# Kernel tuning notes

Hardware: AMD Instinct MI355X
Metric: run time of the kernel (lower is better)

Reference implementation:

```python
import jax, jax.numpy as jnp
import numpy as np

B, NQ, NKV = 4, 1024, 2048
DQ, DC, DI, H = 1024, 1024, 1024, 16
DH = DI // H
EPS = 1e-5


def layer_norm(x, gamma, beta):
    mu = jnp.mean(x, axis=-1, keepdims=True)
    var = jnp.var(x, axis=-1, keepdims=True)
    return (x - mu) * jax.lax.rsqrt(var + EPS) * gamma + beta


def setup_inputs() -> dict:
    key = jax.random.key(0)
    ks = jax.random.split(key, 6)
    s = 0.02
    return {
        "q": jax.random.normal(ks[0], (B, NQ, DQ), jnp.float32),
        "context": jax.random.normal(ks[1], (B, NKV, DC), jnp.float32),
        "Wq": jax.random.normal(ks[2], (DI, DQ), jnp.float32) * s,
        "Wkv": jax.random.normal(ks[3], (2 * DI, DC), jnp.float32) * s,
        "Wproj": jax.random.normal(ks[4], (DQ, DI), jnp.float32) * s,
        "bproj": jnp.zeros((DQ,), jnp.float32),
        "q_gamma": jnp.ones((DQ,), jnp.float32),
        "q_beta": jnp.zeros((DQ,), jnp.float32),
        "c_gamma": jnp.ones((DC,), jnp.float32),
        "c_beta": jnp.zeros((DC,), jnp.float32),
    }


def reference(q, context, Wq, Wkv, Wproj, bproj, q_gamma, q_beta, c_gamma, c_beta):
    scale = DH ** -0.5
    qn = layer_norm(q, q_gamma, q_beta)            # [b, nq, dq]
    cn = layer_norm(context, c_gamma, c_beta)      # [b, nkv, dc]
    qp = qn @ Wq.T                                  # [b, nq, di]
    kv = cn @ Wkv.T                                 # [b, nkv, 2*di]
    k, v = kv[..., :DI], kv[..., DI:]
    qh = qp.reshape(B, NQ, H, DH)
    kh = k.reshape(B, NKV, H, DH)
    vh = v.reshape(B, NKV, H, DH)
    attn = jnp.einsum('bnhd,bmhd->bhnm', qh, kh) * scale   # [b,h,nq,nkv]
    attn = jax.nn.softmax(attn, axis=-1)
    out = jnp.einsum('bhnm,bmhd->bnhd', attn, vh).reshape(B, NQ, DI)
    return out @ Wproj.T + bproj
```

## Files before the change

### kernel.cpp

```cpp
#include <hip/hip_runtime.h>
#include <hip/hip_bf16.h>
#include <stdint.h>

#define B_N 4
#define NQ 1024
#define NKV 2048
#define DI 1024
#define H 16
#define DH 64

using bf16 = __bf16;
typedef bf16 bf16x8 __attribute__((ext_vector_type(8)));
typedef bf16 bf16x4 __attribute__((ext_vector_type(4)));
typedef float f32x4 __attribute__((ext_vector_type(4)));

typedef const __attribute__((address_space(1))) void* gptr_t;
typedef __attribute__((address_space(3))) void* sptr_t;

__global__ __launch_bounds__(256) void prep_kernel(
    const float* __restrict__ q, const float* __restrict__ ctx,
    const float* __restrict__ qg, const float* __restrict__ qb,
    const float* __restrict__ cg, const float* __restrict__ cb,
    bf16* __restrict__ qn, bf16* __restrict__ cn,
    const float* __restrict__ Wq, const float* __restrict__ Wkv, const float* __restrict__ Wproj,
    bf16* __restrict__ oq, bf16* __restrict__ okv, bf16* __restrict__ op) {
  const int blk = blockIdx.x;
  const int t = threadIdx.x;
  if (blk >= 12288) {
    int i = (blk - 12288) * 256 + t;
    const float* src; bf16* dst; int j;
    if (i < 262144)      { src = Wq;    dst = oq;  j = i; }
    else if (i < 786432) { src = Wkv;   dst = okv; j = i - 262144; }
    else                 { src = Wproj; dst = op;  j = i - 786432; }
    float4 v = reinterpret_cast<const float4*>(src)[j];
    bf16x4 o;
    o[0] = (bf16)v.x; o[1] = (bf16)v.y; o[2] = (bf16)v.z; o[3] = (bf16)v.w;
    reinterpret_cast<bf16x4*>(dst)[j] = o;
    return;
  }
  const float* x; const float* gamma; const float* beta; bf16* out; int r;
  if (blk < 4096) { x = q;   gamma = qg; beta = qb; out = qn; r = blk; }
  else            { x = ctx; gamma = cg; beta = cb; out = cn; r = blk - 4096; }
  const float4 v = reinterpret_cast<const float4*>(x + (size_t)r * 1024)[t];
  float s = v.x + v.y + v.z + v.w;
  float s2 = v.x*v.x + v.y*v.y + v.z*v.z + v.w*v.w;
#pragma unroll
  for (int m = 1; m < 64; m <<= 1) { s += __shfl_xor(s, m); s2 += __shfl_xor(s2, m); }
  __shared__ float red[8];
  int wid = t >> 6;
  if ((t & 63) == 0) { red[wid] = s; red[wid + 4] = s2; }
  __syncthreads();
  float ts  = red[0] + red[1] + red[2] + red[3];
  float ts2 = red[4] + red[5] + red[6] + red[7];
  float mean = ts * (1.0f / 1024.0f);
  float var  = ts2 * (1.0f / 1024.0f) - mean * mean;
  float rstd = rsqrtf(var + 1e-5f);
  float4 g  = reinterpret_cast<const float4*>(gamma)[t];
  float4 bb = reinterpret_cast<const float4*>(beta)[t];
  bf16x4 o;
  o[0] = (bf16)((v.x - mean) * rstd * g.x + bb.x);
  o[1] = (bf16)((v.y - mean) * rstd * g.y + bb.y);
  o[2] = (bf16)((v.z - mean) * rstd * g.z + bb.z);
  o[3] = (bf16)((v.w - mean) * rstd * g.w + bb.w);
  reinterpret_cast<bf16x4*>(out + (size_t)r * 1024)[t] = o;
}

template<int MODE, int BN>
__device__ __forceinline__ void gemm_body(bf16* lA, bf16* lB,
    const bf16* __restrict__ A, const bf16* __restrict__ Bm,
    void* __restrict__ out0, void* __restrict__ out1,
    const float* __restrict__ bias, int M, int N, int bid) {
  constexpr int K = 1024;
  constexpr int MI = (BN == 128) ? 4 : 2;
  constexpr int NBL = (BN == 128) ? 4 : 2;
  const int nbn = N / BN;
  const int bm = bid / nbn, bn = bid - bm * nbn;
  const int m0 = bm << 7, n0 = bn * BN;
  const int tid = threadIdx.x;
  const int lane = tid & 63, wid = tid >> 6;
  const int rowb = (BN == 128) ? ((wid >> 1) * 64) : (wid * 32);
  const int colb = (BN == 128) ? ((wid & 1) * 64) : 0;
  const int l15 = lane & 15, lg = lane >> 4;

  f32x4 acc[MI][4] = {};

  const bf16* gA[4]; const bf16* gB[NBL];
#pragma unroll
  for (int u = 0; u < 4; ++u) {
    int s = tid + u * 256;
    int row = s >> 3, c8 = (s & 7) ^ (row & 7);
    gA[u] = A + (size_t)(m0 + row) * K + c8 * 8;
  }
#pragma unroll
  for (int u = 0; u < NBL; ++u) {
    int s = tid + u * 256;
    int row = s >> 3, c8 = (s & 7) ^ (row & 7);
    gB[u] = Bm + (size_t)(n0 + row) * K + c8 * 8;
  }

  const int sw = l15 & 7;

  for (int k0 = 0; k0 < K; k0 += 64) {
#pragma unroll
    for (int u = 0; u < 4; ++u)
      __builtin_amdgcn_global_load_lds((gptr_t)(gA[u] + k0), (sptr_t)(lA + (tid + u * 256) * 8), 16, 0, 0);
#pragma unroll
    for (int u = 0; u < NBL; ++u)
      __builtin_amdgcn_global_load_lds((gptr_t)(gB[u] + k0), (sptr_t)(lB + (tid + u * 256) * 8), 16, 0, 0);
    __syncthreads();
#pragma unroll
    for (int ks2 = 0; ks2 < 2; ++ks2) {
      const int soff = ((ks2 * 4 + lg) ^ sw) * 8;
      bf16x8 af[MI], bfr[4];
#pragma unroll
      for (int i = 0; i < MI; ++i)
        af[i]  = *reinterpret_cast<const bf16x8*>(lA + (rowb + i * 16 + l15) * 64 + soff);
#pragma unroll
      for (int j = 0; j < 4; ++j)
        bfr[j] = *reinterpret_cast<const bf16x8*>(lB + (colb + j * 16 + l15) * 64 + soff);
#pragma unroll
      for (int i = 0; i < MI; ++i)
#pragma unroll
        for (int j = 0; j < 4; ++j)
          acc[i][j] = __builtin_amdgcn_mfma_f32_16x16x32_bf16(af[i], bfr[j], acc[i][j], 0, 0, 0);
    }
    __syncthreads();
  }

  const int mB = m0 + rowb + lg * 4;
  const int nB = n0 + colb + l15;
  if constexpr (MODE == 0) {
    bf16* o = reinterpret_cast<bf16*>(out0);
    constexpr float SC = 0.125f * 1.44269504089f;
#pragma unroll
    for (int i = 0; i < MI; ++i)
#pragma unroll
      for (int j = 0; j < 4; ++j)
#pragma unroll
        for (int r = 0; r < 4; ++r)
          o[(size_t)(mB + i * 16 + r) * N + nB + j * 16] = (bf16)(acc[i][j][r] * SC);
  } else if constexpr (MODE == 2) {
    float* o = reinterpret_cast<float*>(out0);
#pragma unroll
    for (int j = 0; j < 4; ++j) {
      float bj = bias[nB + j * 16];
#pragma unroll
      for (int i = 0; i < MI; ++i)
#pragma unroll
        for (int r = 0; r < 4; ++r)
          o[(size_t)(mB + i * 16 + r) * N + nB + j * 16] = acc[i][j][r] + bj;
    }
  } else {
    if (n0 < 1024) {
      bf16* o = reinterpret_cast<bf16*>(out0);
#pragma unroll
      for (int i = 0; i < MI; ++i)
#pragma unroll
        for (int j = 0; j < 4; ++j)
#pragma unroll
          for (int r = 0; r < 4; ++r)
            o[(size_t)(mB + i * 16 + r) * 1024 + nB + j * 16] = (bf16)acc[i][j][r];
    } else {
      bf16* o = reinterpret_cast<bf16*>(out1);
#pragma unroll
      for (int i = 0; i < MI; ++i) {
        int m = mB + i * 16;
        int bb_ = m >> 11, kv = m & 2047;
        int u = kv & 63;
        int c = (u & 32) | ((u & 12) << 1) | ((u & 16) >> 2) | (u & 3);
        int col = (kv & ~63) | c;
#pragma unroll
        for (int j = 0; j < 4; ++j) {
          int nv = nB + j * 16 - 1024;
          bf16x4 pk;
          pk[0] = (bf16)acc[i][j][0]; pk[1] = (bf16)acc[i][j][1];
          pk[2] = (bf16)acc[i][j][2]; pk[3] = (bf16)acc[i][j][3];
          *reinterpret_cast<bf16x4*>(o + ((size_t)(bb_ << 10) + nv) * 2048 + col) = pk;
        }
      }
    }
  }
}

__global__ __launch_bounds__(256) void gemm_fused(
    const bf16* __restrict__ qn, const bf16* __restrict__ Wq, void* __restrict__ qpb,
    const bf16* __restrict__ cn, const bf16* __restrict__ Wkv,
    void* __restrict__ kbuf, void* __restrict__ vT) {
  __shared__ bf16 lA[128 * 64];
  __shared__ bf16 lB[128 * 64];
  if (blockIdx.x < 1024) {
    int rb = blockIdx.x;
    int bid = (rb & 7) * 128 + (rb >> 3);
    gemm_body<1, 128>(lA, lB, cn, Wkv, kbuf, vT, nullptr, 8192, 2048, bid);
  } else {
    int rb = blockIdx.x - 1024;
    int bid = (rb & 7) * 32 + (rb >> 3);
    gemm_body<0, 128>(lA, lB, qn, Wq, qpb, nullptr, nullptr, 4096, 1024, bid);
  }
}

__global__ __launch_bounds__(256) void gemm_proj(const bf16* __restrict__ A,
    const bf16* __restrict__ Bm, float* __restrict__ out0,
    const float* __restrict__ bias, int M, int N) {
  constexpr int K = 1024;
  __shared__ bf16 lA[128 * 64];
  __shared__ bf16 lB[64 * 64];
  const int cpx = gridDim.x >> 3;
  const int bid = (blockIdx.x & 7) * cpx + (blockIdx.x >> 3);
  const int nbn = N >> 6;
  const int bm = bid / nbn, bn = bid - bm * nbn;
  const int m0 = bm << 7, n0 = bn << 6;
  const int tid = threadIdx.x;
  const int lane = tid & 63, wid = tid >> 6;
  const int rowb = wid * 32;
  const int l15 = lane & 15, lg = lane >> 4;

  f32x4 acc[2][4] = {};

  const bf16* gA[4]; const bf16* gB[2];
#pragma unroll
  for (int u = 0; u < 4; ++u) {
    int s = tid + u * 256;
    int row = s >> 3, c8 = (s & 7) ^ (row & 7);
    gA[u] = A + (size_t)(m0 + row) * K + c8 * 8;
  }
#pragma unroll
  for (int u = 0; u < 2; ++u) {
    int s = tid + u * 256;
    int row = s >> 3, c8 = (s & 7) ^ (row & 7);
    gB[u] = Bm + (size_t)(n0 + row) * K + c8 * 8;
  }
  const int sw = l15 & 7;

  for (int k0 = 0; k0 < K; k0 += 64) {
#pragma unroll
    for (int u = 0; u < 4; ++u)
      __builtin_amdgcn_global_load_lds((gptr_t)(gA[u] + k0), (sptr_t)(lA + (tid + u * 256) * 8), 16, 0, 0);
#pragma unroll
    for (int u = 0; u < 2; ++u)
      __builtin_amdgcn_global_load_lds((gptr_t)(gB[u] + k0), (sptr_t)(lB + (tid + u * 256) * 8), 16, 0, 0);
    __syncthreads();
#pragma unroll
    for (int ks2 = 0; ks2 < 2; ++ks2) {
      const int soff = ((ks2 * 4 + lg) ^ sw) * 8;
      bf16x8 af[2], bfr[4];
#pragma unroll
      for (int i = 0; i < 2; ++i)
        af[i]  = *reinterpret_cast<const bf16x8*>(lA + (rowb + i * 16 + l15) * 64 + soff);
#pragma unroll
      for (int j = 0; j < 4; ++j)
        bfr[j] = *reinterpret_cast<const bf16x8*>(lB + (j * 16 + l15) * 64 + soff);
#pragma unroll
      for (int i = 0; i < 2; ++i)
#pragma unroll
        for (int j = 0; j < 4; ++j)
          acc[i][j] = __builtin_amdgcn_mfma_f32_16x16x32_bf16(af[i], bfr[j], acc[i][j], 0, 0, 0);
    }
    __syncthreads();
  }

  const int mB = m0 + rowb + lg * 4;
  const int nB = n0 + l15;
#pragma unroll
  for (int j = 0; j < 4; ++j) {
    float bj = bias[nB + j * 16];
#pragma unroll
    for (int i = 0; i < 2; ++i)
#pragma unroll
      for (int r = 0; r < 4; ++r)
        out0[(size_t)(mB + i * 16 + r) * N + nB + j * 16] = acc[i][j][r] + bj;
  }
}

__global__ __launch_bounds__(512, 4) void attn_kernel(const bf16* __restrict__ qp,
    const bf16* __restrict__ kk, const bf16* __restrict__ vTp, bf16* __restrict__ out) {
  __shared__ bf16 smem[32768];
  const int pos = blockIdx.x;
  const int idx = pos >> 3;
  const int bh = ((idx >> 3) << 3) | (pos & 7);
  const int qt = idx & 7;
  const int b = bh >> 4, h = bh & 15;
  const int tid = threadIdx.x;
  const int lane = tid & 63, w = tid >> 6;
  const int l15 = lane & 15, lg = lane >> 4;

  const bf16* Qb = qp + (size_t)(b * NQ + qt * 128 + w * 16) * DI + h * DH;
  const bf16* Kb = kk + (size_t)b * NKV * DI + h * DH;
  const bf16* Vb = vTp + (size_t)(b * DI + h * DH) * NKV;

  const int sA = tid, sB = tid + 512;
  const int rKA = ((sA >> 7) << 4) | (sA & 15), cKA = ((sA >> 4) & 7) * 8;
  const int rKB = ((sB >> 7) << 4) | (sB & 15), cKB = ((sB >> 4) & 7) * 8;
  const int rVA = ((sA >> 8) << 4) | (sA & 15), cVA = ((sA >> 6) & 3) * 32 + ((sA >> 4) & 3) * 8;
  const int rVB = ((sB >> 8) << 4) | (sB & 15), cVB = ((sB >> 6) & 3) * 32 + ((sB >> 4) & 3) * 8;
  const bf16* pKA = Kb + (size_t)rKA * DI + cKA;
  const bf16* pKB = Kb + (size_t)rKB * DI + cKB;
  const bf16* pVA = Vb + (size_t)rVA * NKV + cVA;
  const bf16* pVB = Vb + (size_t)rVB * NKV + cVB;

#define STAGE_KV(bufsel, kv)                                                                        \
  do {                                                                                              \
    __builtin_amdgcn_global_load_lds((gptr_t)(pKA + (size_t)(kv) * DI),                             \
                                     (sptr_t)(smem + (bufsel) * 8192 + sA * 8), 16, 0, 0);          \
    __builtin_amdgcn_global_load_lds((gptr_t)(pKB + (size_t)(kv) * DI),                             \
                                     (sptr_t)(smem + (bufsel) * 8192 + sB * 8), 16, 0, 0);          \
    __builtin_amdgcn_global_load_lds((gptr_t)(pVA + (kv)),                                          \
                                     (sptr_t)(smem + 16384 + (bufsel) * 8192 + sA * 8), 16, 0, 0);  \
    __builtin_amdgcn_global_load_lds((gptr_t)(pVB + (kv)),                                          \
                                     (sptr_t)(smem + 16384 + (bufsel) * 8192 + sB * 8), 16, 0, 0);  \
  } while (0)

  bf16x8 qf[2];
#pragma unroll
  for (int ks = 0; ks < 2; ++ks)
    qf[ks] = *reinterpret_cast<const bf16x8*>(Qb + (size_t)l15 * DI + ks * 32 + lg * 8);

  bf16x8 onesf;
#pragma unroll
  for (int jj = 0; jj < 8; ++jj) onesf[jj] = (bf16)1.0f;

  f32x4 o[4] = {};
  f32x4 lacc = {};
  float mrun = -1e30f;

  STAGE_KV(0, 0);
  __syncthreads();
  int cur = 0;

  for (int kv0 = 0; kv0 < NKV; kv0 += 128) {
    const bool notlast = (kv0 + 128 < NKV);
    if (notlast) STAGE_KV(cur ^ 1, kv0 + 128);

    const bf16* Kl = smem + cur * 8192;
    const bf16* Vl = smem + 16384 + cur * 8192;

    f32x4 s[8] = {};
#pragma unroll
    for (int h2 = 0; h2 < 2; ++h2) {
      bf16x8 kf[4][2];
#pragma unroll
      for (int ni = 0; ni < 4; ++ni)
#pragma unroll
        for (int ks = 0; ks < 2; ++ks)
          kf[ni][ks] = *reinterpret_cast<const bf16x8*>(Kl + (((h2 * 4 + ni) * 2 + ks) * 64 + lane) * 8);
      __builtin_amdgcn_s_setprio(1);
#pragma unroll
      for (int ni = 0; ni < 4; ++ni)
#pragma unroll
        for (int ks = 0; ks < 2; ++ks)
          s[h2 * 4 + ni] = __builtin_amdgcn_mfma_f32_16x16x32_bf16(kf[ni][ks], qf[ks], s[h2 * 4 + ni], 0, 0, 0);
      __builtin_amdgcn_s_setprio(0);
    }

    float pmr[4];
#pragma unroll
    for (int r = 0; r < 4; ++r) {
      float a = fmaxf(fmaxf(s[0][r], s[1][r]), s[2][r]);
      a = fmaxf(fmaxf(a, s[3][r]), s[4][r]);
      a = fmaxf(fmaxf(a, s[5][r]), s[6][r]);
      pmr[r] = fmaxf(a, s[7][r]);
    }
    float pm = fmaxf(fmaxf(pmr[0], pmr[1]), fmaxf(pmr[2], pmr[3]));
    pm = fmaxf(pm, __shfl_xor(pm, 16));
    pm = fmaxf(pm, __shfl_xor(pm, 32));

    const bool noresc = __all(pm <= mrun);
    const float mnew = noresc ? mrun : fmaxf(mrun, pm);

#pragma unroll
    for (int i = 0; i < 8; ++i)
#pragma unroll
      for (int r = 0; r < 4; ++r)
        s[i][r] = __builtin_amdgcn_exp2f(s[i][r] - mnew);

    if (!noresc) {
      float corr = __builtin_amdgcn_exp2f(mrun - mnew);
      mrun = mnew;
      float c0 = __shfl(corr, lg * 4 + 0);
      float c1 = __shfl(corr, lg * 4 + 1);
      float c2 = __shfl(corr, lg * 4 + 2);
      float c3 = __shfl(corr, lg * 4 + 3);
      lacc[0] *= c0; lacc[1] *= c1; lacc[2] *= c2; lacc[3] *= c3;
#pragma unroll
      for (int dt = 0; dt < 4; ++dt) {
        o[dt][0] *= c0; o[dt][1] *= c1; o[dt][2] *= c2; o[dt][3] *= c3;
      }
    }

    bf16x8 pa[4];
#pragma unroll
    for (int h2 = 0; h2 < 2; ++h2)
#pragma unroll
      for (int k2p = 0; k2p < 2; ++k2p)
#pragma unroll
        for (int jj = 0; jj < 4; ++jj) {
          pa[h2 * 2 + k2p][jj]     = (bf16)s[h2 * 4 + k2p * 2 + 0][jj];
          pa[h2 * 2 + k2p][4 + jj] = (bf16)s[h2 * 4 + k2p * 2 + 1][jj];
        }

    __builtin_amdgcn_s_setprio(1);
#pragma unroll
    for (int k2 = 0; k2 < 4; ++k2) {
      bf16x8 vf[4];
#pragma unroll
      for (int dt = 0; dt < 4; ++dt)
        vf[dt] = *reinterpret_cast<const bf16x8*>(Vl + ((dt * 4 + k2) * 64 + lane) * 8);
#pragma unroll
      for (int dt = 0; dt < 4; ++dt)
        o[dt] = __builtin_amdgcn_mfma_f32_16x16x32_bf16(pa[k2], vf[dt], o[dt], 0, 0, 0);
      lacc = __builtin_amdgcn_mfma_f32_16x16x32_bf16(pa[k2], onesf, lacc, 0, 0, 0);
    }
    __builtin_amdgcn_s_setprio(0);

    if (notlast) __syncthreads();
    cur ^= 1;
  }
#undef STAGE_KV

  const float iv0 = 1.0f / lacc[0];
  const float iv1 = 1.0f / lacc[1];
  const float iv2 = 1.0f / lacc[2];
  const float iv3 = 1.0f / lacc[3];

  bf16* Ob = out + (size_t)(b * NQ + qt * 128 + w * 16) * DI + h * DH;
#pragma unroll
  for (int dt = 0; dt < 4; ++dt) {
    Ob[(size_t)(lg * 4 + 0) * DI + dt * 16 + l15] = (bf16)(o[dt][0] * iv0);
    Ob[(size_t)(lg * 4 + 1) * DI + dt * 16 + l15] = (bf16)(o[dt][1] * iv1);
    Ob[(size_t)(lg * 4 + 2) * DI + dt * 16 + l15] = (bf16)(o[dt][2] * iv2);
    Ob[(size_t)(lg * 4 + 3) * DI + dt * 16 + l15] = (bf16)(o[dt][3] * iv3);
  }
}

extern "C" void kernel_launch(void* const* d_in, const int* in_sizes, int n_in,
                              void* d_out, int out_size, void* d_ws, size_t ws_size,
                              hipStream_t stream) {
  const float* q     = (const float*)d_in[0];
  const float* ctx   = (const float*)d_in[1];
  const float* Wq    = (const float*)d_in[2];
  const float* Wkv   = (const float*)d_in[3];
  const float* Wproj = (const float*)d_in[4];
  const float* bproj = (const float*)d_in[5];
  const float* qg    = (const float*)d_in[6];
  const float* qb    = (const float*)d_in[7];
  const float* cg    = (const float*)d_in[8];
  const float* cb    = (const float*)d_in[9];

  char* ws = (char*)d_ws;
  bf16* qn    = (bf16*)(ws);
  bf16* cn    = (bf16*)(ws + ( 8ull << 20));
  bf16* Wq_b  = (bf16*)(ws + (24ull << 20));
  bf16* Wkv_b = (bf16*)(ws + (26ull << 20));
  bf16* Wp_b  = (bf16*)(ws + (30ull << 20));
  bf16* qpb   = (bf16*)(ws + (32ull << 20));
  bf16* kbuf  = (bf16*)(ws + (40ull << 20));
  bf16* vT    = (bf16*)(ws + (56ull << 20));
  bf16* aout  = (bf16*)(ws + (72ull << 20));

  prep_kernel<<<16384, 256, 0, stream>>>(q, ctx, qg, qb, cg, cb, qn, cn,
                                         Wq, Wkv, Wproj, Wq_b, Wkv_b, Wp_b);

  gemm_fused<<<1280, 256, 0, stream>>>(qn, Wq_b, qpb, cn, Wkv_b, kbuf, vT);

  attn_kernel<<<512, 512, 0, stream>>>(qpb, kbuf, vT, aout);

  gemm_proj<<<512, 256, 0, stream>>>(aout, Wp_b, (float*)d_out, bproj, 4096, 1024);
}
```

Baseline: 139.2 us.

## Double-buffer LDS tiles in fused QKV GEMM with async prefetch

```diff
diff --git a/kernel.cpp b/kernel.cpp
--- a/kernel.cpp
+++ b/kernel.cpp
@@ -65,67 +65,76 @@
   reinterpret_cast<bf16x4*>(out + (size_t)r * 1024)[t] = o;
 }
 
-template<int MODE, int BN>
-__device__ __forceinline__ void gemm_body(bf16* lA, bf16* lB,
+template<int MODE>
+__device__ __forceinline__ void gemm_db_body(bf16* lA, bf16* lB,
     const bf16* __restrict__ A, const bf16* __restrict__ Bm,
-    void* __restrict__ out0, void* __restrict__ out1,
-    const float* __restrict__ bias, int M, int N, int bid) {
+    void* __restrict__ out0, void* __restrict__ out1, int N, int bid) {
   constexpr int K = 1024;
-  constexpr int MI = (BN == 128) ? 4 : 2;
-  constexpr int NBL = (BN == 128) ? 4 : 2;
-  const int nbn = N / BN;
+  const int nbn = N >> 7;
   const int bm = bid / nbn, bn = bid - bm * nbn;
-  const int m0 = bm << 7, n0 = bn * BN;
+  const int m0 = bm << 7, n0 = bn << 7;
   const int tid = threadIdx.x;
   const int lane = tid & 63, wid = tid >> 6;
-  const int rowb = (BN == 128) ? ((wid >> 1) * 64) : (wid * 32);
-  const int colb = (BN == 128) ? ((wid & 1) * 64) : 0;
+  const int rowb = (wid >> 1) * 64, colb = (wid & 1) * 64;
   const int l15 = lane & 15, lg = lane >> 4;
 
-  f32x4 acc[MI][4] = {};
-
-  const bf16* gA[4]; const bf16* gB[NBL];
+  f32x4 acc[4][4] = {};
+
+  const bf16* gA[4]; const bf16* gB[4];
 #pragma unroll
   for (int u = 0; u < 4; ++u) {
     int s = tid + u * 256;
     int row = s >> 3, c8 = (s & 7) ^ (row & 7);
     gA[u] = A + (size_t)(m0 + row) * K + c8 * 8;
-  }
-#pragma unroll
-  for (int u = 0; u < NBL; ++u) {
-    int s = tid + u * 256;
-    int row = s >> 3, c8 = (s & 7) ^ (row & 7);
     gB[u] = Bm + (size_t)(n0 + row) * K + c8 * 8;
   }
-
   const int sw = l15 & 7;
 
-  for (int k0 = 0; k0 < K; k0 += 64) {
-#pragma unroll
-    for (int u = 0; u < 4; ++u)
-      __builtin_amdgcn_global_load_lds((gptr_t)(gA[u] + k0), (sptr_t)(lA + (tid + u * 256) * 8), 16, 0, 0);
-#pragma unroll
-    for (int u = 0; u < NBL; ++u)
-      __builtin_amdgcn_global_load_lds((gptr_t)(gB[u] + k0), (sptr_t)(lB + (tid + u * 256) * 8), 16, 0, 0);
-    __syncthreads();
+#define DBSTAGE(buf, k0)                                                                             \
+  do {                                                                                               \
+    _Pragma("unroll")                                                                                \
+    for (int u = 0; u < 4; ++u)                                                                      \
+      __builtin_amdgcn_global_load_lds((gptr_t)(gA[u] + (k0)),                                       \
+          (sptr_t)(lA + (buf) * 8192 + (tid + u * 256) * 8), 16, 0, 0);                              \
+    _Pragma("unroll")                                                                                \
+    for (int u = 0; u < 4; ++u)                                                                      \
+      __builtin_amdgcn_global_load_lds((gptr_t)(gB[u] + (k0)),                                       \
+          (sptr_t)(lB + (buf) * 8192 + (tid + u * 256) * 8), 16, 0, 0);                              \
+  } while (0)
+
+  DBSTAGE(0, 0);
+
+  for (int kt = 0; kt < 16; ++kt) {
+    const int cur = kt & 1;
+    __builtin_amdgcn_s_barrier();
+    if (kt < 15) {
+      DBSTAGE(cur ^ 1, (kt + 1) * 64);
+      asm volatile("s_waitcnt vmcnt(8)" ::: "memory");
+    } else {
+      asm volatile("s_waitcnt vmcnt(0)" ::: "memory");
+    }
+    const bf16* lAc = lA + cur * 8192;
+    const bf16* lBc = lB + cur * 8192;
 #pragma unroll
     for (int ks2 = 0; ks2 < 2; ++ks2) {
       const int soff = ((ks2 * 4 + lg) ^ sw) * 8;
-      bf16x8 af[MI], bfr[4];
-#pragma unroll
-      for (int i = 0; i < MI; ++i)
-        af[i]  = *reinterpret_cast<const bf16x8*>(lA + (rowb + i * 16 + l15) * 64 + soff);
+      bf16x8 af[4], bfr[4];
+#pragma unroll
+      for (int i = 0; i < 4; ++i)
+        af[i]  = *reinterpret_cast<const bf16x8*>(lAc + (rowb + i * 16 + l15) * 64 + soff);
 #pragma unroll
       for (int j = 0; j < 4; ++j)
-        bfr[j] = *reinterpret_cast<const bf16x8*>(lB + (colb + j * 16 + l15) * 64 + soff);
-#pragma unroll
-      for (int i = 0; i < MI; ++i)
+        bfr[j] = *reinterpret_cast<const bf16x8*>(lBc + (colb + j * 16 + l15) * 64 + soff);
+      __builtin_amdgcn_s_setprio(1);
+#pragma unroll
+      for (int i = 0; i < 4; ++i)
 #pragma unroll
         for (int j = 0; j < 4; ++j)
           acc[i][j] = __builtin_amdgcn_mfma_f32_16x16x32_bf16(af[i], bfr[j], acc[i][j], 0, 0, 0);
-    }
-    __syncthreads();
-  }
+      __builtin_amdgcn_s_setprio(0);
+    }
+  }
+#undef DBSTAGE
 
   const int mB = m0 + rowb + lg * 4;
   const int nB = n0 + colb + l15;
@@ -133,28 +142,17 @@
     bf16* o = reinterpret_cast<bf16*>(out0);
     constexpr float SC = 0.125f * 1.44269504089f;
 #pragma unroll
-    for (int i = 0; i < MI; ++i)
+    for (int i = 0; i < 4; ++i)
 #pragma unroll
       for (int j = 0; j < 4; ++j)
 #pragma unroll
         for (int r = 0; r < 4; ++r)
           o[(size_t)(mB + i * 16 + r) * N + nB + j * 16] = (bf16)(acc[i][j][r] * SC);
-  } else if constexpr (MODE == 2) {
-    float* o = reinterpret_cast<float*>(out0);
-#pragma unroll
-    for (int j = 0; j < 4; ++j) {
-      float bj = bias[nB + j * 16];
-#pragma unroll
-      for (int i = 0; i < MI; ++i)
-#pragma unroll
-        for (int r = 0; r < 4; ++r)
-          o[(size_t)(mB + i * 16 + r) * N + nB + j * 16] = acc[i][j][r] + bj;
-    }
   } else {
     if (n0 < 1024) {
       bf16* o = reinterpret_cast<bf16*>(out0);
 #pragma unroll
-      for (int i = 0; i < MI; ++i)
+      for (int i = 0; i < 4; ++i)
 #pragma unroll
         for (int j = 0; j < 4; ++j)
 #pragma unroll
@@ -163,7 +161,7 @@
     } else {
       bf16* o = reinterpret_cast<bf16*>(out1);
 #pragma unroll
-      for (int i = 0; i < MI; ++i) {
+      for (int i = 0; i < 4; ++i) {
         int m = mB + i * 16;
         int bb_ = m >> 11, kv = m & 2047;
         int u = kv & 63;
@@ -186,16 +184,16 @@
     const bf16* __restrict__ qn, const bf16* __restrict__ Wq, void* __restrict__ qpb,
     const bf16* __restrict__ cn, const bf16* __restrict__ Wkv,
     void* __restrict__ kbuf, void* __restrict__ vT) {
-  __shared__ bf16 lA[128 * 64];
-  __shared__ bf16 lB[128 * 64];
+  __shared__ bf16 lA[2 * 8192];
+  __shared__ bf16 lB[2 * 8192];
   if (blockIdx.x < 1024) {
     int rb = blockIdx.x;
     int bid = (rb & 7) * 128 + (rb >> 3);
-    gemm_body<1, 128>(lA, lB, cn, Wkv, kbuf, vT, nullptr, 8192, 2048, bid);
+    gemm_db_body<1>(lA, lB, cn, Wkv, kbuf, vT, 2048, bid);
   } else {
     int rb = blockIdx.x - 1024;
     int bid = (rb & 7) * 32 + (rb >> 3);
-    gemm_body<0, 128>(lA, lB, qn, Wq, qpb, nullptr, nullptr, 4096, 1024, bid);
+    gemm_db_body<0>(lA, lB, qn, Wq, qpb, nullptr, 1024, bid);
   }
 }
 
```

After: 143.0 us. 1.03x slower.
